# Optimization experiments

Measured on AMD Instinct MI355X. Metric: run time of the kernel, lower is better.

The kernel has to match this reference:

```python
import jax, jax.numpy as jnp
import numpy as np
from jax import lax

EPS = 1e-5

def ste_sign(x):
    # forward-only module: plain sign is fine
    return jnp.sign(x)

def conv2d(x, w, pad):
    # x: NCHW, w: OIHW, stride 1
    return lax.conv_general_dilated(x, w, window_strides=(1, 1),
                                    padding=[(pad, pad), (pad, pad)],
                                    dimension_numbers=('NCHW', 'OIHW', 'NCHW'))

def maxpool2(x):
    # 2x2 max pool, stride 2, VALID (floor) -- matches nn.MaxPool2d(2,2)
    return lax.reduce_window(x, -jnp.inf, lax.max, (1, 1, 2, 2), (1, 1, 2, 2), 'VALID')

def batchnorm(x, gamma, beta):
    # training-mode BN: batch statistics over (N,H,W), biased variance
    mean = jnp.mean(x, axis=(0, 2, 3), keepdims=True)
    var = jnp.var(x, axis=(0, 2, 3), keepdims=True)
    xn = (x - mean) * lax.rsqrt(var + EPS)
    return xn * gamma[None, :, None, None] + beta[None, :, None, None]

def setup_inputs() -> dict:
    key = jax.random.key(0)
    ks = jax.random.split(key, 8)
    def he(k, shape):
        n = shape[2] * shape[3] * shape[0]
        return jax.random.normal(k, shape, jnp.float32) * np.sqrt(2.0 / n)
    x = jax.random.normal(ks[0], (4096, 1, 28, 28), jnp.float32)
    w0 = he(ks[1], (32, 1, 3, 3))
    w1 = he(ks[2], (32, 32, 3, 3))
    w2 = he(ks[3], (32, 32, 3, 3))
    g0 = jnp.ones((32,), jnp.float32); b0 = jnp.zeros((32,), jnp.float32)
    g1 = jnp.ones((32,), jnp.float32); b1 = jnp.zeros((32,), jnp.float32)
    g2 = jnp.ones((32,), jnp.float32); b2 = jnp.zeros((32,), jnp.float32)
    fw = jax.random.normal(ks[4], (10, 288), jnp.float32) * 0.01
    fb = jnp.zeros((10,), jnp.float32)
    return {"x": x, "w0": w0, "g0": g0, "b0": b0, "w1": w1, "g1": g1, "b1": b1,
            "w2": w2, "g2": g2, "b2": b2, "fw": fw, "fb": fb}

def reference(x, w0, g0, b0, w1, g1, b1, w2, g2, b2, fw, fb):
    # block0: fp conv -> pool -> bn (no act)
    h = batchnorm(maxpool2(conv2d(x, w0, 1)), g0, b0)          # [B,32,14,14]
    # block1: binary(1w1a) conv -> pool -> bn + maxpool(shortcut)
    o = batchnorm(maxpool2(conv2d(ste_sign(h), ste_sign(w1), 1)), g1, b1)
    h = o + maxpool2(h)                                         # [B,32,7,7]
    # block2
    o = batchnorm(maxpool2(conv2d(ste_sign(h), ste_sign(w2), 1)), g2, b2)
    h = o + maxpool2(h)                                         # [B,32,3,3]
    h = h.reshape(h.shape[0], -1)                                # [B,288]
    return h @ fw.T + fb                                         # [B,10]
```

## Files before the change

kernel.cpp:

```cpp
#include <hip/hip_runtime.h>
#include <stdint.h>

#define BATCH 4096

typedef float v16f __attribute__((ext_vector_type(16)));
typedef short v8s  __attribute__((ext_vector_type(8)));

__global__ __launch_bounds__(448) void k_conv0f2(const float* __restrict__ x,
                                                 const float* __restrict__ w0,
                                                 const float* __restrict__ w1,
                                                 const float* __restrict__ w2,
                                                 uint16_t* __restrict__ w1f,
                                                 uint16_t* __restrict__ w2f,
                                                 double* __restrict__ part0,
                                                 float* __restrict__ mg) {
    __shared__ float xsA[960], xsB[960];
    __shared__ float wl[288];
    __shared__ double rs[896], rq[896];
    int t = threadIdx.x;
    int nA = blockIdx.x * 2, nB = nA + 1;

    if (blockIdx.x < 72 && t < 256) {
        int i = blockIdx.x * 256 + t;
        int ii = (i < 9216) ? i : i - 9216;
        const float* w = (i < 9216) ? w1 : w2;
        uint16_t* o = (i < 9216) ? w1f : w2f;
        int j = ii & 7, nn = (ii >> 3) & 31, q2 = (ii >> 8) & 1, kh = (ii >> 9) & 1, tp = ii >> 10;
        int cin = kh * 16 + q2 * 8 + j;
        float v = w[(nn * 32 + cin) * 9 + tp];
        o[ii] = (v > 0.f) ? 0x3F80 : ((v < 0.f) ? 0xBF80 : 0);
    }

    for (int i = t; i < 960; i += 448) { xsA[i] = 0.f; xsB[i] = 0.f; }
    for (int i = t; i < 288; i += 448) wl[i] = w0[i];
    __syncthreads();
    for (int i = t; i < 784; i += 448) {
        int y = i / 28, xx = i - y * 28;
        xsA[(y + 1) * 32 + xx + 1] = x[nA * 784 + i];
        xsB[(y + 1) * 32 + xx + 1] = x[nB * 784 + i];
    }
    __syncthreads();
    int c = t & 31, py = t >> 5;
    float wreg[9];
    #pragma unroll
    for (int i = 0; i < 9; ++i) wreg[i] = wl[c * 9 + i];
    const float4* XA = (const float4*)xsA;
    const float4* XB = (const float4*)xsB;
    float4 cA0 = XA[(2 * py + 0) * 8];
    float4 cA1 = XA[(2 * py + 1) * 8];
    float4 cA2 = XA[(2 * py + 2) * 8];
    float4 cA3 = XA[(2 * py + 3) * 8];
    float4 cB0 = XB[(2 * py + 0) * 8];
    float4 cB1 = XB[(2 * py + 1) * 8];
    float4 cB2 = XB[(2 * py + 2) * 8];
    float4 cB3 = XB[(2 * py + 3) * 8];
    float* mrA = mg + (size_t)nA * 6272;
    float* mrB = mg + (size_t)nB * 6272;
    double sA = 0.0, qA = 0.0, sB = 0.0, qB = 0.0;
    #pragma unroll
    for (int k = 0; k < 7; ++k) {
        float4 nA0 = XA[(2 * py + 0) * 8 + k + 1];
        float4 nA1 = XA[(2 * py + 1) * 8 + k + 1];
        float4 nA2 = XA[(2 * py + 2) * 8 + k + 1];
        float4 nA3 = XA[(2 * py + 3) * 8 + k + 1];
        float4 nB0 = XB[(2 * py + 0) * 8 + k + 1];
        float4 nB1 = XB[(2 * py + 1) * 8 + k + 1];
        float4 nB2 = XB[(2 * py + 2) * 8 + k + 1];
        float4 nB3 = XB[(2 * py + 3) * 8 + k + 1];
        float aA[4][6], aB[4][6];
        aA[0][0] = cA0.x; aA[0][1] = cA0.y; aA[0][2] = cA0.z; aA[0][3] = cA0.w; aA[0][4] = nA0.x; aA[0][5] = nA0.y;
        aA[1][0] = cA1.x; aA[1][1] = cA1.y; aA[1][2] = cA1.z; aA[1][3] = cA1.w; aA[1][4] = nA1.x; aA[1][5] = nA1.y;
        aA[2][0] = cA2.x; aA[2][1] = cA2.y; aA[2][2] = cA2.z; aA[2][3] = cA2.w; aA[2][4] = nA2.x; aA[2][5] = nA2.y;
        aA[3][0] = cA3.x; aA[3][1] = cA3.y; aA[3][2] = cA3.z; aA[3][3] = cA3.w; aA[3][4] = nA3.x; aA[3][5] = nA3.y;
        aB[0][0] = cB0.x; aB[0][1] = cB0.y; aB[0][2] = cB0.z; aB[0][3] = cB0.w; aB[0][4] = nB0.x; aB[0][5] = nB0.y;
        aB[1][0] = cB1.x; aB[1][1] = cB1.y; aB[1][2] = cB1.z; aB[1][3] = cB1.w; aB[1][4] = nB1.x; aB[1][5] = nB1.y;
        aB[2][0] = cB2.x; aB[2][1] = cB2.y; aB[2][2] = cB2.z; aB[2][3] = cB2.w; aB[2][4] = nB2.x; aB[2][5] = nB2.y;
        aB[3][0] = cB3.x; aB[3][1] = cB3.y; aB[3][2] = cB3.z; aB[3][3] = cB3.w; aB[3][4] = nB3.x; aB[3][5] = nB3.y;
        #pragma unroll
        for (int e = 0; e < 2; ++e) {
            int base = 2 * e;
            float sA00 = 0.f, sA01 = 0.f, sA10 = 0.f, sA11 = 0.f;
            float sB00 = 0.f, sB01 = 0.f, sB10 = 0.f, sB11 = 0.f;
            #pragma unroll
            for (int ky = 0; ky < 3; ++ky)
            #pragma unroll
            for (int kx = 0; kx < 3; ++kx) {
                float w = wreg[ky * 3 + kx];
                sA00 = fmaf(aA[ky][base + kx], w, sA00);
                sA01 = fmaf(aA[ky][base + kx + 1], w, sA01);
                sA10 = fmaf(aA[ky + 1][base + kx], w, sA10);
                sA11 = fmaf(aA[ky + 1][base + kx + 1], w, sA11);
                sB00 = fmaf(aB[ky][base + kx], w, sB00);
                sB01 = fmaf(aB[ky][base + kx + 1], w, sB01);
                sB10 = fmaf(aB[ky + 1][base + kx], w, sB10);
                sB11 = fmaf(aB[ky + 1][base + kx + 1], w, sB11);
            }
            float mA = fmaxf(fmaxf(sA00, sA01), fmaxf(sA10, sA11));
            float mB = fmaxf(fmaxf(sB00, sB01), fmaxf(sB10, sB11));
            int pix = py * 14 + 2 * k + e;
            mrA[pix * 32 + c] = mA;
            mrB[pix * 32 + c] = mB;
            double vA = (double)mA, vB = (double)mB;
            sA += vA; qA += vA * vA;
            sB += vB; qB += vB * vB;
        }
        cA0 = nA0; cA1 = nA1; cA2 = nA2; cA3 = nA3;
        cB0 = nB0; cB1 = nB1; cB2 = nB2; cB3 = nB3;
    }
    rs[c * 14 + py] = sA; rq[c * 14 + py] = qA;
    rs[448 + c * 14 + py] = sB; rq[448 + c * 14 + py] = qB;
    __syncthreads();
    if (t < 32) {
        double SA = 0.0, QA = 0.0;
        #pragma unroll
        for (int i = 0; i < 14; ++i) { SA += rs[t * 14 + i]; QA += rq[t * 14 + i]; }
        part0[(size_t)t * 4096 + nA] = SA;
        part0[(size_t)32 * 4096 + (size_t)t * 4096 + nA] = QA;
        double SB = 0.0, QB = 0.0;
        #pragma unroll
        for (int i = 0; i < 14; ++i) { SB += rs[448 + t * 14 + i]; QB += rq[448 + t * 14 + i]; }
        part0[(size_t)t * 4096 + nB] = SB;
        part0[(size_t)32 * 4096 + (size_t)t * 4096 + nB] = QB;
    }
}

__global__ __launch_bounds__(256) void k_finalize(const double* __restrict__ part, int G,
                                                  const float* __restrict__ g,
                                                  const float* __restrict__ b,
                                                  double inv_count, float* __restrict__ ss) {
    int c = blockIdx.x, t = threadIdx.x;
    double s = 0.0, q = 0.0;
    for (int i = t; i < G; i += 256) {
        s += part[(size_t)c * G + i];
        q += part[(size_t)32 * G + (size_t)c * G + i];
    }
    #pragma unroll
    for (int o = 32; o > 0; o >>= 1) { s += __shfl_down(s, o); q += __shfl_down(q, o); }
    __shared__ double rs[4], rq[4];
    int w = t >> 6, l = t & 63;
    if (l == 0) { rs[w] = s; rq[w] = q; }
    __syncthreads();
    if (t == 0) {
        s = rs[0] + rs[1] + rs[2] + rs[3];
        q = rq[0] + rq[1] + rq[2] + rq[3];
        double mean = s * inv_count;
        double var = q * inv_count - mean * mean;
        double sc = (double)g[c] / sqrt(var + 1e-5);
        ss[c] = (float)sc;
        ss[32 + c] = (float)((double)b[c] - mean * sc);
    }
}

__global__ __launch_bounds__(256) void k_conv1s(const float* __restrict__ m,
                                                const float* __restrict__ ss,
                                                const uint16_t* __restrict__ w1f,
                                                float* __restrict__ p1,
                                                double* __restrict__ part1) {
    __shared__ uint32_t lds[8192];
    int t = threadIdx.x;
    int n0 = blockIdx.x * 2;
    int lane = t & 63, wv = t >> 6;
    int q = lane >> 5, ncol = lane & 31;
    v8s wfr[18];
    #pragma unroll
    for (int f = 0; f < 18; ++f)
        wfr[f] = *(const v8s*)(w1f + (f * 2 + q) * 256 + ncol * 8);

    uint4 z4; z4.x = z4.y = z4.z = z4.w = 0u;
    for (int i = t; i < 480; i += 256) {
        int img = (i >= 240) ? 1 : 0;
        int e2 = i - img * 240;
        int e = e2 >> 2, qd = e2 & 3;
        int yh, xh;
        if (e < 16)      { yh = 0;      xh = e; }
        else if (e < 32) { yh = 15;     xh = e - 16; }
        else if (e < 46) { yh = e - 31; xh = 0; }
        else             { yh = e - 45; xh = 15; }
        *(uint4*)&lds[img * 4096 + (yh * 16 + xh) * 16 + qd * 4] = z4;
    }
    int u = t >> 2, tq = t & 3;
    float sc8[8], sh8[8];
    #pragma unroll
    for (int j = 0; j < 8; ++j) { sc8[j] = ss[tq * 8 + j]; sh8[j] = ss[32 + tq * 8 + j]; }
    for (int pg = u; pg < 392; pg += 64) {
        int img = (pg >= 196) ? 1 : 0;
        int pl = pg - img * 196;
        int iy = pl / 14, ix = pl - iy * 14;
        int yy = iy + 1, xx2 = ix + 1;
        int p = yy * 16 + xx2;
        int psw = (xx2 & 3) ^ (yy & 3);
        int qd = tq ^ psw;
        const float4* mp = (const float4*)(m + ((size_t)(n0 + img) * 196 + pl) * 32 + tq * 8);
        float4 v0 = mp[0], v1 = mp[1];
        float h[8];
        h[0] = fmaf(sc8[0], v0.x, sh8[0]); h[1] = fmaf(sc8[1], v0.y, sh8[1]);
        h[2] = fmaf(sc8[2], v0.z, sh8[2]); h[3] = fmaf(sc8[3], v0.w, sh8[3]);
        h[4] = fmaf(sc8[4], v1.x, sh8[4]); h[5] = fmaf(sc8[5], v1.y, sh8[5]);
        h[6] = fmaf(sc8[6], v1.z, sh8[6]); h[7] = fmaf(sc8[7], v1.w, sh8[7]);
        uint32_t d[4];
        #pragma unroll
        for (int j = 0; j < 4; ++j) {
            float h0 = h[2 * j], h1 = h[2 * j + 1];
            uint32_t b0 = (h0 > 0.f) ? 0x3F80u : ((h0 < 0.f) ? 0xBF80u : 0u);
            uint32_t b1 = (h1 > 0.f) ? 0x3F80u : ((h1 < 0.f) ? 0xBF80u : 0u);
            d[j] = b0 | (b1 << 16);
        }
        uint4 v; v.x = d[0]; v.y = d[1]; v.z = d[2]; v.w = d[3];
        *(uint4*)&lds[img * 4096 + p * 16 + qd * 4] = v;
    }
    __syncthreads();

    int img = wv >> 1, wh = wv & 1;
    int n = n0 + img;
    int ibase = img * 4096;
    int mm = lane & 31;
    int quad = mm & 3, pwl = mm >> 2;
    int dy = quad >> 1, dx = quad & 1;
    double sAcc = 0.0, qAcc = 0.0;
    for (int tile = wh; tile < 7; tile += 2) {
        int pw = tile * 8 + pwl;
        int pwc = min(pw, 48);
        int py = pwc / 7, px = pwc - py * 7;
        int pbase = (2 * py + dy) * 16 + 2 * px + dx;
        v16f acc;
        #pragma unroll
        for (int i = 0; i < 16; ++i) acc[i] = 0.f;
        #pragma unroll
        for (int tp = 0; tp < 9; ++tp) {
            int p = pbase + (tp / 3) * 16 + (tp % 3);
            int psw = (p ^ (p >> 4)) & 3;
            #pragma unroll
            for (int kh = 0; kh < 2; ++kh) {
                int g = kh * 2 + q;
                int idx = ibase + p * 16 + ((g ^ psw) << 2);
                v8s a = *(const v8s*)&lds[idx];
                acc = __builtin_amdgcn_mfma_f32_32x32x16_bf16(a, wfr[tp * 2 + kh], acc, 0, 0, 0);
            }
        }
        #pragma unroll
        for (int g4 = 0; g4 < 4; ++g4) {
            float mx = fmaxf(fmaxf(acc[4 * g4], acc[4 * g4 + 1]),
                             fmaxf(acc[4 * g4 + 2], acc[4 * g4 + 3]));
            int pwo = tile * 8 + 2 * g4 + q;
            if (pwo < 49) {
                p1[((size_t)n * 49 + pwo) * 32 + ncol] = mx;
                double v = (double)mx;
                sAcc += v; qAcc += v * v;
            }
        }
    }
    __syncthreads();
    double* red = (double*)lds;
    red[(wv * 2 + q) * 32 + ncol] = sAcc;
    red[256 + (wv * 2 + q) * 32 + ncol] = qAcc;
    __syncthreads();
    if (t < 32) {
        double S = 0.0, Q = 0.0;
        #pragma unroll
        for (int i = 0; i < 8; ++i) { S += red[i * 32 + t]; Q += red[256 + i * 32 + t]; }
        part1[(size_t)t * 2048 + blockIdx.x] = S;
        part1[(size_t)32 * 2048 + (size_t)t * 2048 + blockIdx.x] = Q;
    }
}

__global__ __launch_bounds__(256) void k_bc2m(const float* __restrict__ p1,
                                              const float* __restrict__ m,
                                              const float* __restrict__ ss,
                                              const uint16_t* __restrict__ w2f,
                                              float* __restrict__ p2,
                                              float* __restrict__ hp1,
                                              double* __restrict__ part2) {
    __shared__ uint32_t lds[8192];
    __shared__ float Htmp[1568];
    int t = threadIdx.x;
    int n0 = blockIdx.x * 8;
    int lane = t & 63, wv = t >> 6;
    int q = lane >> 5, ncol = lane & 31;

    int cb = t & 7;
    float sc1v[4], sh1v[4], sc0v[4], sh0v[4];
    #pragma unroll
    for (int j = 0; j < 4; ++j) {
        sc1v[j] = ss[64 + cb * 4 + j]; sh1v[j] = ss[96 + cb * 4 + j];
        sc0v[j] = ss[cb * 4 + j];      sh0v[j] = ss[32 + cb * 4 + j];
    }
    int pw0 = t >> 3;
    int py0 = pw0 / 7, px0 = pw0 - py0 * 7;
    int mb0 = ((2 * py0) * 14 + 2 * px0) * 8 + cb;
    int pw1 = 32 + (t >> 3);
    int py1 = pw1 / 7, px1 = pw1 - py1 * 7;
    int mb1 = ((2 * py1) * 14 + 2 * px1) * 8 + cb;

    float4 pa, pb, a0, a1, a2, a3, b0_, b1_, b2_, b3_;
    {
        const float4* P4 = (const float4*)(p1 + (size_t)n0 * 1568);
        const float4* M4 = (const float4*)(m + (size_t)n0 * 6272);
        pa = P4[t];
        a0 = M4[mb0]; a1 = M4[mb0 + 8]; a2 = M4[mb0 + 112]; a3 = M4[mb0 + 120];
        if (t < 136) {
            pb = P4[256 + t];
            b0_ = M4[mb1]; b1_ = M4[mb1 + 8]; b2_ = M4[mb1 + 112]; b3_ = M4[mb1 + 120];
        }
    }

    float4* Ht4 = (float4*)Htmp;
    for (int img = 0; img < 8; ++img) {
        float4 npa, npb, na0, na1, na2, na3, nb0, nb1, nb2, nb3;
        if (img < 7) {
            const float4* P4 = (const float4*)(p1 + (size_t)(n0 + img + 1) * 1568);
            const float4* M4 = (const float4*)(m + (size_t)(n0 + img + 1) * 6272);
            npa = P4[t];
            na0 = M4[mb0]; na1 = M4[mb0 + 8]; na2 = M4[mb0 + 112]; na3 = M4[mb0 + 120];
            if (t < 136) {
                npb = P4[256 + t];
                nb0 = M4[mb1]; nb1 = M4[mb1 + 8]; nb2 = M4[mb1 + 112]; nb3 = M4[mb1 + 120];
            }
        }
        if (img) __syncthreads();
        {
            float mx0 = fmaxf(fmaxf(a0.x, a1.x), fmaxf(a2.x, a3.x));
            float mx1 = fmaxf(fmaxf(a0.y, a1.y), fmaxf(a2.y, a3.y));
            float mx2 = fmaxf(fmaxf(a0.z, a1.z), fmaxf(a2.z, a3.z));
            float mx3 = fmaxf(fmaxf(a0.w, a1.w), fmaxf(a2.w, a3.w));
            float mn0 = fminf(fminf(a0.x, a1.x), fminf(a2.x, a3.x));
            float mn1 = fminf(fminf(a0.y, a1.y), fminf(a2.y, a3.y));
            float mn2 = fminf(fminf(a0.z, a1.z), fminf(a2.z, a3.z));
            float mn3 = fminf(fminf(a0.w, a1.w), fminf(a2.w, a3.w));
            float s0 = (sc0v[0] > 0.f) ? mx0 : mn0;
            float s1 = (sc0v[1] > 0.f) ? mx1 : mn1;
            float s2 = (sc0v[2] > 0.f) ? mx2 : mn2;
            float s3 = (sc0v[3] > 0.f) ? mx3 : mn3;
            float4 hv;
            hv.x = fmaf(sc1v[0], pa.x, sh1v[0]) + fmaf(sc0v[0], s0, sh0v[0]);
            hv.y = fmaf(sc1v[1], pa.y, sh1v[1]) + fmaf(sc0v[1], s1, sh0v[1]);
            hv.z = fmaf(sc1v[2], pa.z, sh1v[2]) + fmaf(sc0v[2], s2, sh0v[2]);
            hv.w = fmaf(sc1v[3], pa.w, sh1v[3]) + fmaf(sc0v[3], s3, sh0v[3]);
            Ht4[t] = hv;
            if (t < 136) {
                float ux0 = fmaxf(fmaxf(b0_.x, b1_.x), fmaxf(b2_.x, b3_.x));
                float ux1 = fmaxf(fmaxf(b0_.y, b1_.y), fmaxf(b2_.y, b3_.y));
                float ux2 = fmaxf(fmaxf(b0_.z, b1_.z), fmaxf(b2_.z, b3_.z));
                float ux3 = fmaxf(fmaxf(b0_.w, b1_.w), fmaxf(b2_.w, b3_.w));
                float un0 = fminf(fminf(b0_.x, b1_.x), fminf(b2_.x, b3_.x));
                float un1 = fminf(fminf(b0_.y, b1_.y), fminf(b2_.y, b3_.y));
                float un2 = fminf(fminf(b0_.z, b1_.z), fminf(b2_.z, b3_.z));
                float un3 = fminf(fminf(b0_.w, b1_.w), fminf(b2_.w, b3_.w));
                float u0 = (sc0v[0] > 0.f) ? ux0 : un0;
                float u1 = (sc0v[1] > 0.f) ? ux1 : un1;
                float u2 = (sc0v[2] > 0.f) ? ux2 : un2;
                float u3 = (sc0v[3] > 0.f) ? ux3 : un3;
                float4 hw;
                hw.x = fmaf(sc1v[0], pb.x, sh1v[0]) + fmaf(sc0v[0], u0, sh0v[0]);
                hw.y = fmaf(sc1v[1], pb.y, sh1v[1]) + fmaf(sc0v[1], u1, sh0v[1]);
                hw.z = fmaf(sc1v[2], pb.z, sh1v[2]) + fmaf(sc0v[2], u2, sh0v[2]);
                hw.w = fmaf(sc1v[3], pb.w, sh1v[3]) + fmaf(sc0v[3], u3, sh0v[3]);
                Ht4[256 + t] = hw;
            }
        }
        __syncthreads();
        uint32_t* ap = &lds[img * 1024];
        #pragma unroll
        for (int ii = 0; ii < 4; ++ii) {
            int i = t + ii * 256;
            int pp = i >> 4, r = i & 15;
            int y = pp >> 3, xq = pp & 7;
            uint32_t d = 0u;
            if (y >= 1 && xq >= 1) {
                int pix = (y - 1) * 7 + (xq - 1);
                int sub = r & 3;
                int g = (r >> 2) ^ (pp & 3);
                int c0 = ((g << 2) | sub) * 2;
                float h0 = Htmp[pix * 32 + c0];
                float h1 = Htmp[pix * 32 + c0 + 1];
                uint32_t w0b = (h0 > 0.f) ? 0x3F80u : ((h0 < 0.f) ? 0xBF80u : 0u);
                uint32_t w1b = (h1 > 0.f) ? 0x3F80u : ((h1 < 0.f) ? 0xBF80u : 0u);
                d = w0b | (w1b << 16);
            }
            ap[i] = d;
        }
        for (int jj = t; jj < 288; jj += 256) {
            int c = jj / 9, pix = jj - c * 9;
            int r = pix / 3, qq = pix - r * 3;
            float e0 = Htmp[((2 * r) * 7 + 2 * qq) * 32 + c];
            float e1 = Htmp[((2 * r) * 7 + 2 * qq + 1) * 32 + c];
            float e2 = Htmp[((2 * r + 1) * 7 + 2 * qq) * 32 + c];
            float e3 = Htmp[((2 * r + 1) * 7 + 2 * qq + 1) * 32 + c];
            hp1[(size_t)(n0 + img) * 288 + c * 9 + pix] = fmaxf(fmaxf(e0, e1), fmaxf(e2, e3));
        }
        pa = npa; pb = npb;
        a0 = na0; a1 = na1; a2 = na2; a3 = na3;
        b0_ = nb0; b1_ = nb1; b2_ = nb2; b3_ = nb3;
    }
    __syncthreads();

    v8s wfr[18];
    #pragma unroll
    for (int f = 0; f < 18; ++f)
        wfr[f] = *(const v8s*)(w2f + (f * 2 + q) * 256 + ncol * 8);

    int mmm = lane & 31;
    int quad = mmm & 3, pwl = mmm >> 2;
    int dy = quad >> 1, dx = quad & 1;
    double sAcc = 0.0, qAcc = 0.0;
    for (int tile = wv; tile < 9; tile += 4) {
        int pwg = tile * 8 + pwl;
        int img = pwg / 9, pwi = pwg - img * 9;
        int py = pwi / 3, px = pwi - py * 3;
        int pbase = (2 * py + dy) * 8 + 2 * px + dx;
        v16f acc;
        #pragma unroll
        for (int i = 0; i < 16; ++i) acc[i] = 0.f;
        #pragma unroll
        for (int tp = 0; tp < 9; ++tp) {
            int p = pbase + (tp / 3) * 8 + (tp % 3);
            int psw = p & 3;
            #pragma unroll
            for (int kh = 0; kh < 2; ++kh) {
                int g = kh * 2 + q;
                int idx = img * 1024 + p * 16 + ((g ^ psw) << 2);
                v8s a = *(const v8s*)&lds[idx];
                acc = __builtin_amdgcn_mfma_f32_32x32x16_bf16(a, wfr[tp * 2 + kh], acc, 0, 0, 0);
            }
        }
        #pragma unroll
        for (int g4 = 0; g4 < 4; ++g4) {
            float mx = fmaxf(fmaxf(acc[4 * g4], acc[4 * g4 + 1]),
                             fmaxf(acc[4 * g4 + 2], acc[4 * g4 + 3]));
            int pwo = tile * 8 + 2 * g4 + q;
            int oimg = pwo / 9, opwi = pwo - oimg * 9;
            p2[(size_t)(n0 + oimg) * 288 + ncol * 9 + opwi] = mx;
            double v = (double)mx;
            sAcc += v; qAcc += v * v;
        }
    }
    __syncthreads();
    double* red = (double*)lds;
    red[(wv * 2 + q) * 32 + ncol] = sAcc;
    red[256 + (wv * 2 + q) * 32 + ncol] = qAcc;
    __syncthreads();
    if (t < 32) {
        double S = 0.0, Q = 0.0;
        #pragma unroll
        for (int i = 0; i < 8; ++i) { S += red[i * 32 + t]; Q += red[256 + i * 32 + t]; }
        part2[(size_t)t * 512 + blockIdx.x] = S;
        part2[(size_t)32 * 512 + (size_t)t * 512 + blockIdx.x] = Q;
    }
}

__global__ __launch_bounds__(256) void k_fc(const float* __restrict__ p2,
                                            const float* __restrict__ hp1,
                                            const float* __restrict__ ss,
                                            const float* __restrict__ fw,
                                            const float* __restrict__ fb,
                                            float* __restrict__ outv) {
    int wv = threadIdx.x >> 6, l = threadIdx.x & 63;
    int n = blockIdx.x * 4 + wv;
    float acc[10];
    #pragma unroll
    for (int k = 0; k < 10; ++k) acc[k] = 0.f;
    #pragma unroll
    for (int i = 0; i < 5; ++i) {
        int j = l + 64 * i;
        if (j < 288) {
            int c = j / 9;
            float h = fmaf(ss[128 + c], p2[n * 288 + j], ss[160 + c]) + hp1[n * 288 + j];
            #pragma unroll
            for (int k = 0; k < 10; ++k)
                acc[k] = fmaf(h, fw[k * 288 + j], acc[k]);
        }
    }
    #pragma unroll
    for (int k = 0; k < 10; ++k) {
        float s = acc[k];
        #pragma unroll
        for (int o = 32; o > 0; o >>= 1) s += __shfl_down(s, o);
        if (l == 0) outv[n * 10 + k] = s + fb[k];
    }
}

extern "C" void kernel_launch(void* const* d_in, const int* in_sizes, int n_in,
                              void* d_out, int out_size, void* d_ws, size_t ws_size,
                              hipStream_t stream) {
    (void)in_sizes; (void)n_in; (void)out_size; (void)ws_size;
    const float* x  = (const float*)d_in[0];
    const float* w0 = (const float*)d_in[1];
    const float* g0 = (const float*)d_in[2];
    const float* b0 = (const float*)d_in[3];
    const float* w1 = (const float*)d_in[4];
    const float* g1 = (const float*)d_in[5];
    const float* b1 = (const float*)d_in[6];
    const float* w2 = (const float*)d_in[7];
    const float* g2 = (const float*)d_in[8];
    const float* b2 = (const float*)d_in[9];
    const float* fw = (const float*)d_in[10];
    const float* fb = (const float*)d_in[11];
    float* outv = (float*)d_out;
    char* ws = (char*)d_ws;

    float*     ss    = (float*)(ws + 1024);
    uint16_t*  w1f   = (uint16_t*)(ws + 2048);
    uint16_t*  w2f   = (uint16_t*)(ws + 20480);
    double*    part1 = (double*)(ws + 38912);
    double*    part0 = (double*)(ws + 1087488);
    float*     p1    = (float*)(ws + 3184640);
    float*     p2    = (float*)(ws + 28874752);
    float*     hp1   = (float*)(ws + 33593344);
    double*    part2 = (double*)(ws + 38311936);
    float*     m     = (float*)(ws + 38574080);

    k_conv0f2<<<BATCH / 2, 448, 0, stream>>>(x, w0, w1, w2, w1f, w2f, part0, m);
    k_finalize<<<32, 256, 0, stream>>>(part0, 4096, g0, b0, 1.0 / (BATCH * 196.0), ss);

    k_conv1s<<<BATCH / 2, 256, 0, stream>>>(m, ss, w1f, p1, part1);
    k_finalize<<<32, 256, 0, stream>>>(part1, 2048, g1, b1, 1.0 / (BATCH * 49.0), ss + 64);

    k_bc2m<<<BATCH / 8, 256, 0, stream>>>(p1, m, ss, w2f, p2, hp1, part2);
    k_finalize<<<32, 256, 0, stream>>>(part2, 512, g2, b2, 1.0 / (BATCH * 9.0), ss + 128);

    k_fc<<<BATCH / 4, 256, 0, stream>>>(p2, hp1, ss, fw, fb, outv);
}
```

Before: 186.1 us.

## Precompute shortcut 2x2 max/min pools in conv0 and read them in block2

The first conv kernel now also produces the 2x2-pooled max and min of the pre-BN block0 output, using a cross-half-wave shuffle, and writes them to two new buffers. The block2 kernel reads these compact pooled arrays instead of gathering four strided values from the full 14x14 map for every pooled pixel. This cuts the strided global reads in k_bc2m. In exchange, conv0 writes two extra arrays and does extra shuffles, so the total memory written grows.

```diff
diff --git a/kernel.cpp b/kernel.cpp
--- a/kernel.cpp
+++ b/kernel.cpp
@@ -13,7 +13,9 @@
                                                  uint16_t* __restrict__ w1f,
                                                  uint16_t* __restrict__ w2f,
                                                  double* __restrict__ part0,
-                                                 float* __restrict__ mg) {
+                                                 float* __restrict__ mg,
+                                                 float* __restrict__ pm,
+                                                 float* __restrict__ pmin) {
     __shared__ float xsA[960], xsB[960];
     __shared__ float wl[288];
     __shared__ double rs[896], rq[896];
@@ -57,6 +59,7 @@
     float* mrA = mg + (size_t)nA * 6272;
     float* mrB = mg + (size_t)nB * 6272;
     double sA = 0.0, qA = 0.0, sB = 0.0, qB = 0.0;
+    float pA0 = 0.f, pB0 = 0.f;
     #pragma unroll
     for (int k = 0; k < 7; ++k) {
         float4 nA0 = XA[(2 * py + 0) * 8 + k + 1];
@@ -103,6 +106,22 @@
             double vA = (double)mA, vB = (double)mB;
             sA += vA; qA += vA * vA;
             sB += vB; qB += vB * vB;
+            if (e == 0) { pA0 = mA; pB0 = mB; }
+            else {
+                float cxA = fmaxf(pA0, mA), cnA = fminf(pA0, mA);
+                float cxB = fmaxf(pB0, mB), cnB = fminf(pB0, mB);
+                float xxA = fmaxf(cxA, __shfl_xor(cxA, 32));
+                float nnA = fminf(cnA, __shfl_xor(cnA, 32));
+                float xxB = fmaxf(cxB, __shfl_xor(cxB, 32));
+                float nnB = fminf(cnB, __shfl_xor(cnB, 32));
+                if (!(py & 1)) {
+                    int pw = (py >> 1) * 7 + k;
+                    pm[(size_t)nA * 1568 + pw * 32 + c] = xxA;
+                    pmin[(size_t)nA * 1568 + pw * 32 + c] = nnA;
+                    pm[(size_t)nB * 1568 + pw * 32 + c] = xxB;
+                    pmin[(size_t)nB * 1568 + pw * 32 + c] = nnB;
+                }
+            }
         }
         cA0 = nA0; cA1 = nA1; cA2 = nA2; cA3 = nA3;
         cB0 = nB0; cB1 = nB1; cB2 = nB2; cB3 = nB3;
@@ -264,7 +283,8 @@
 }
 
 __global__ __launch_bounds__(256) void k_bc2m(const float* __restrict__ p1,
-                                              const float* __restrict__ m,
+                                              const float* __restrict__ pm,
+                                              const float* __restrict__ pmin,
                                               const float* __restrict__ ss,
                                               const uint16_t* __restrict__ w2f,
                                               float* __restrict__ p2,
@@ -284,52 +304,32 @@
         sc1v[j] = ss[64 + cb * 4 + j]; sh1v[j] = ss[96 + cb * 4 + j];
         sc0v[j] = ss[cb * 4 + j];      sh0v[j] = ss[32 + cb * 4 + j];
     }
-    int pw0 = t >> 3;
-    int py0 = pw0 / 7, px0 = pw0 - py0 * 7;
-    int mb0 = ((2 * py0) * 14 + 2 * px0) * 8 + cb;
-    int pw1 = 32 + (t >> 3);
-    int py1 = pw1 / 7, px1 = pw1 - py1 * 7;
-    int mb1 = ((2 * py1) * 14 + 2 * px1) * 8 + cb;
-
-    float4 pa, pb, a0, a1, a2, a3, b0_, b1_, b2_, b3_;
+
+    float4 pa, pb, ma, mb, na, nb;
     {
         const float4* P4 = (const float4*)(p1 + (size_t)n0 * 1568);
-        const float4* M4 = (const float4*)(m + (size_t)n0 * 6272);
-        pa = P4[t];
-        a0 = M4[mb0]; a1 = M4[mb0 + 8]; a2 = M4[mb0 + 112]; a3 = M4[mb0 + 120];
-        if (t < 136) {
-            pb = P4[256 + t];
-            b0_ = M4[mb1]; b1_ = M4[mb1 + 8]; b2_ = M4[mb1 + 112]; b3_ = M4[mb1 + 120];
-        }
+        const float4* M4 = (const float4*)(pm + (size_t)n0 * 1568);
+        const float4* N4 = (const float4*)(pmin + (size_t)n0 * 1568);
+        pa = P4[t]; ma = M4[t]; na = N4[t];
+        if (t < 136) { pb = P4[256 + t]; mb = M4[256 + t]; nb = N4[256 + t]; }
     }
 
     float4* Ht4 = (float4*)Htmp;
     for (int img = 0; img < 8; ++img) {
-        float4 npa, npb, na0, na1, na2, na3, nb0, nb1, nb2, nb3;
+        float4 npa, npb, nma, nmb, nna, nnb;
         if (img < 7) {
             const float4* P4 = (const float4*)(p1 + (size_t)(n0 + img + 1) * 1568);
-            const float4* M4 = (const float4*)(m + (size_t)(n0 + img + 1) * 6272);
-            npa = P4[t];
-            na0 = M4[mb0]; na1 = M4[mb0 + 8]; na2 = M4[mb0 + 112]; na3 = M4[mb0 + 120];
-            if (t < 136) {
-                npb = P4[256 + t];
-                nb0 = M4[mb1]; nb1 = M4[mb1 + 8]; nb2 = M4[mb1 + 112]; nb3 = M4[mb1 + 120];
-            }
+            const float4* M4 = (const float4*)(pm + (size_t)(n0 + img + 1) * 1568);
+            const float4* N4 = (const float4*)(pmin + (size_t)(n0 + img + 1) * 1568);
+            npa = P4[t]; nma = M4[t]; nna = N4[t];
+            if (t < 136) { npb = P4[256 + t]; nmb = M4[256 + t]; nnb = N4[256 + t]; }
         }
         if (img) __syncthreads();
         {
-            float mx0 = fmaxf(fmaxf(a0.x, a1.x), fmaxf(a2.x, a3.x));
-            float mx1 = fmaxf(fmaxf(a0.y, a1.y), fmaxf(a2.y, a3.y));
-            float mx2 = fmaxf(fmaxf(a0.z, a1.z), fmaxf(a2.z, a3.z));
-            float mx3 = fmaxf(fmaxf(a0.w, a1.w), fmaxf(a2.w, a3.w));
-            float mn0 = fminf(fminf(a0.x, a1.x), fminf(a2.x, a3.x));
-            float mn1 = fminf(fminf(a0.y, a1.y), fminf(a2.y, a3.y));
-            float mn2 = fminf(fminf(a0.z, a1.z), fminf(a2.z, a3.z));
-            float mn3 = fminf(fminf(a0.w, a1.w), fminf(a2.w, a3.w));
-            float s0 = (sc0v[0] > 0.f) ? mx0 : mn0;
-            float s1 = (sc0v[1] > 0.f) ? mx1 : mn1;
-            float s2 = (sc0v[2] > 0.f) ? mx2 : mn2;
-            float s3 = (sc0v[3] > 0.f) ? mx3 : mn3;
+            float s0 = (sc0v[0] > 0.f) ? ma.x : na.x;
+            float s1 = (sc0v[1] > 0.f) ? ma.y : na.y;
+            float s2 = (sc0v[2] > 0.f) ? ma.z : na.z;
+            float s3 = (sc0v[3] > 0.f) ? ma.w : na.w;
             float4 hv;
             hv.x = fmaf(sc1v[0], pa.x, sh1v[0]) + fmaf(sc0v[0], s0, sh0v[0]);
             hv.y = fmaf(sc1v[1], pa.y, sh1v[1]) + fmaf(sc0v[1], s1, sh0v[1]);
@@ -337,18 +337,10 @@
             hv.w = fmaf(sc1v[3], pa.w, sh1v[3]) + fmaf(sc0v[3], s3, sh0v[3]);
             Ht4[t] = hv;
             if (t < 136) {
-                float ux0 = fmaxf(fmaxf(b0_.x, b1_.x), fmaxf(b2_.x, b3_.x));
-                float ux1 = fmaxf(fmaxf(b0_.y, b1_.y), fmaxf(b2_.y, b3_.y));
-                float ux2 = fmaxf(fmaxf(b0_.z, b1_.z), fmaxf(b2_.z, b3_.z));
-                float ux3 = fmaxf(fmaxf(b0_.w, b1_.w), fmaxf(b2_.w, b3_.w));
-                float un0 = fminf(fminf(b0_.x, b1_.x), fminf(b2_.x, b3_.x));
-                float un1 = fminf(fminf(b0_.y, b1_.y), fminf(b2_.y, b3_.y));
-                float un2 = fminf(fminf(b0_.z, b1_.z), fminf(b2_.z, b3_.z));
-                float un3 = fminf(fminf(b0_.w, b1_.w), fminf(b2_.w, b3_.w));
-                float u0 = (sc0v[0] > 0.f) ? ux0 : un0;
-                float u1 = (sc0v[1] > 0.f) ? ux1 : un1;
-                float u2 = (sc0v[2] > 0.f) ? ux2 : un2;
-                float u3 = (sc0v[3] > 0.f) ? ux3 : un3;
+                float u0 = (sc0v[0] > 0.f) ? mb.x : nb.x;
+                float u1 = (sc0v[1] > 0.f) ? mb.y : nb.y;
+                float u2 = (sc0v[2] > 0.f) ? mb.z : nb.z;
+                float u3 = (sc0v[3] > 0.f) ? mb.w : nb.w;
                 float4 hw;
                 hw.x = fmaf(sc1v[0], pb.x, sh1v[0]) + fmaf(sc0v[0], u0, sh0v[0]);
                 hw.y = fmaf(sc1v[1], pb.y, sh1v[1]) + fmaf(sc0v[1], u1, sh0v[1]);
@@ -387,9 +379,7 @@
             float e3 = Htmp[((2 * r + 1) * 7 + 2 * qq + 1) * 32 + c];
             hp1[(size_t)(n0 + img) * 288 + c * 9 + pix] = fmaxf(fmaxf(e0, e1), fmaxf(e2, e3));
         }
-        pa = npa; pb = npb;
-        a0 = na0; a1 = na1; a2 = na2; a3 = na3;
-        b0_ = nb0; b1_ = nb1; b2_ = nb2; b3_ = nb3;
+        pa = npa; pb = npb; ma = nma; mb = nmb; na = nna; nb = nnb;
     }
     __syncthreads();
 
@@ -506,15 +496,17 @@
     float*     p2    = (float*)(ws + 28874752);
     float*     hp1   = (float*)(ws + 33593344);
     double*    part2 = (double*)(ws + 38311936);
-    float*     m     = (float*)(ws + 38574080);
-
-    k_conv0f2<<<BATCH / 2, 448, 0, stream>>>(x, w0, w1, w2, w1f, w2f, part0, m);
+    float*     pm    = (float*)(ws + 38574080);
+    float*     pmin  = (float*)(ws + 64264192);
+    float*     m     = (float*)(ws + 89954304);
+
+    k_conv0f2<<<BATCH / 2, 448, 0, stream>>>(x, w0, w1, w2, w1f, w2f, part0, m, pm, pmin);
     k_finalize<<<32, 256, 0, stream>>>(part0, 4096, g0, b0, 1.0 / (BATCH * 196.0), ss);
 
     k_conv1s<<<BATCH / 2, 256, 0, stream>>>(m, ss, w1f, p1, part1);
     k_finalize<<<32, 256, 0, stream>>>(part1, 2048, g1, b1, 1.0 / (BATCH * 49.0), ss + 64);
 
-    k_bc2m<<<BATCH / 8, 256, 0, stream>>>(p1, m, ss, w2f, p2, hp1, part2);
+    k_bc2m<<<BATCH / 8, 256, 0, stream>>>(p1, pm, pmin, ss, w2f, p2, hp1, part2);
     k_finalize<<<32, 256, 0, stream>>>(part2, 512, g2, b2, 1.0 / (BATCH * 9.0), ss + 128);
 
     k_fc<<<BATCH / 4, 256, 0, stream>>>(p2, hp1, ss, fw, fb, outv);
```

After: 190.4 us. +2.3%, slower.
